# Kernel tuning notes

Hardware: AMD Instinct MI355X
Metric: run time of the kernel (lower is better)

Reference implementation:

```python
import jax, jax.numpy as jnp
import numpy as np

B, DIM, N = 8, 512, 1024
EMB, CDIM, M = 128, 512, 256
HEADS, DHEAD = 8, 64
DFF = 4 * DIM  # GEGLU inner dim


def _group_norm(x, g, b, groups=32, eps=1e-6):
    # x: [B, C, L]
    Bx, C, L = x.shape
    xr = x.reshape(Bx, groups, (C // groups) * L)
    mu = xr.mean(-1, keepdims=True)
    var = xr.var(-1, keepdims=True)
    xn = ((xr - mu) * jax.lax.rsqrt(var + eps)).reshape(Bx, C, L)
    return xn * g[None, :, None] + b[None, :, None]


def _layer_norm(x, g, b, eps=1e-5):
    mu = x.mean(-1, keepdims=True)
    var = x.var(-1, keepdims=True)
    return (x - mu) * jax.lax.rsqrt(var + eps) * g + b


def _attention(x, ctx, wq, wk, wv, wo, bo, heads):
    # x: [B, Nq, Dq], ctx: [B, Nk, Dk]
    Bx, Nq, _ = x.shape
    q = x @ wq.T
    k = ctx @ wk.T
    v = ctx @ wv.T
    d = q.shape[-1] // heads
    sp = lambda t: t.reshape(Bx, -1, heads, d).transpose(0, 2, 1, 3)  # b h n d
    q, k, v = sp(q), sp(k), sp(v)
    sim = jnp.einsum('bhid,bhjd->bhij', q, k) * (d ** -0.5)
    o = jnp.einsum('bhij,bhjd->bhid', jax.nn.softmax(sim, axis=-1), v)
    o = o.transpose(0, 2, 1, 3).reshape(Bx, Nq, heads * d)
    return o @ wo.T + bo


def setup_inputs() -> dict:
    key = jax.random.key(0)
    ks = jax.random.split(key, 16)
    rn = lambda k, sh: jax.random.normal(k, sh, dtype=jnp.float32) * 0.02
    inner = HEADS * DHEAD
    z = lambda n: jnp.zeros((n,), jnp.float32)
    o = lambda n: jnp.ones((n,), jnp.float32)
    return {
        'x': jax.random.normal(ks[0], (B, DIM, N), dtype=jnp.float32),
        'emb': jax.random.normal(ks[1], (B, EMB), dtype=jnp.float32),
        'context': jax.random.normal(ks[2], (B, CDIM, M), dtype=jnp.float32),
        'w_emb': rn(ks[3], (2 * DIM, EMB)), 'b_emb': z(2 * DIM),
        'gn_g': o(DIM), 'gn_b': z(DIM),
        'conv_w': rn(ks[4], (DIM, DIM)), 'conv_b': z(DIM),
        'a1_wq': rn(ks[5], (inner, DIM)), 'a1_wk': rn(ks[6], (inner, DIM)),
        'a1_wv': rn(ks[7], (inner, DIM)), 'a1_wo': rn(ks[8], (DIM, inner)), 'a1_bo': z(DIM),
        'a2_wq': rn(ks[9], (inner, DIM)), 'a2_wk': rn(ks[10], (inner, CDIM)),
        'a2_wv': rn(ks[11], (inner, CDIM)), 'a2_wo': rn(ks[12], (DIM, inner)), 'a2_bo': z(DIM),
        'ln1_g': o(DIM), 'ln1_b': z(DIM),
        'ln2_g': o(DIM), 'ln2_b': z(DIM),
        'ln3_g': o(DIM), 'ln3_b': z(DIM),
        'ff_w1': rn(ks[13], (2 * DFF, DIM)), 'ff_b1': z(2 * DFF),
        'ff_w2': rn(ks[14], (DIM, DFF)), 'ff_b2': z(DIM),
    }


def reference(x, emb, context, w_emb, b_emb, gn_g, gn_b, conv_w, conv_b,
              a1_wq, a1_wk, a1_wv, a1_wo, a1_bo,
              a2_wq, a2_wk, a2_wv, a2_wo, a2_bo,
              ln1_g, ln1_b, ln2_g, ln2_b, ln3_g, ln3_b,
              ff_w1, ff_b1, ff_w2, ff_b2):
    # scale-shift modulated GroupNorm + SiLU + 1x1 Conv1d residual branch
    emb_out = (jax.nn.silu(emb) @ w_emb.T + b_emb)[:, :, None]  # [B, 2*dim, 1]
    scale, shift = jnp.split(emb_out, 2, axis=1)
    h = _group_norm(x, gn_g, gn_b) * (1.0 + scale) + shift
    h = jnp.einsum('oc,bcn->bon', conv_w, jax.nn.silu(h)) + conv_b[None, :, None]
    x = x + h
    # to token-major layout
    xt = x.transpose(0, 2, 1)          # [B, N, dim]
    ctx = context.transpose(0, 2, 1)   # [B, M, context_dim]
    # self attention
    y = _layer_norm(xt, ln1_g, ln1_b)
    xt = _attention(y, y, a1_wq, a1_wk, a1_wv, a1_wo, a1_bo, HEADS) + xt
    # cross attention
    xt = _attention(_layer_norm(xt, ln2_g, ln2_b), ctx,
                    a2_wq, a2_wk, a2_wv, a2_wo, a2_bo, HEADS) + xt
    # GEGLU feed-forward
    u = _layer_norm(xt, ln3_g, ln3_b) @ ff_w1.T + ff_b1
    a, g = jnp.split(u, 2, axis=-1)
    xt = (a * jax.nn.gelu(g, approximate=False)) @ ff_w2.T + ff_b2 + xt
    return xt.transpose(0, 2, 1)  # back to [B, dim, N]
```

## Files before the change

kernel.cpp:

```cpp
#include <hip/hip_runtime.h>
#include <math.h>

#define NB 8
#define CDIM 512
#define NT 1024
#define MT 256
#define DFFI 2048

typedef short bf16x8 __attribute__((ext_vector_type(8)));
typedef float f32x4 __attribute__((ext_vector_type(4)));

__device__ __forceinline__ float sigmoidf_(float v){ return 1.0f/(1.0f+__expf(-v)); }

__device__ __forceinline__ short f2bf(float f){
    union { float f; unsigned u; } v; v.f = f;
    unsigned r = v.u + 0x7FFFu + ((v.u >> 16) & 1u);
    return (short)(r >> 16);
}

#define GLDS(gp, lp) __builtin_amdgcn_global_load_lds( \
    (const __attribute__((address_space(1))) void*)(gp), \
    (__attribute__((address_space(3))) void*)(lp), 16, 0, 0)

__global__ void cvt_all(const float* __restrict__ a1wq, const float* __restrict__ a1wk,
                        const float* __restrict__ a1wv, const float* __restrict__ a1wo,
                        const float* __restrict__ a2wq, const float* __restrict__ a2wk,
                        const float* __restrict__ a2wv, const float* __restrict__ a2wo,
                        const float* __restrict__ ffw1, const float* __restrict__ ffw2,
                        const float* __restrict__ convw, short* __restrict__ WB){
    int e = (blockIdx.x*256 + threadIdx.x)*8;
    if (e >= 5505024) return;
    const float* src; int off;
    if (e < 2097152){
        const float* tbl[8] = {a1wq,a1wk,a1wv,a1wo,a2wq,a2wk,a2wv,a2wo};
        src = tbl[e >> 18]; off = e & 262143;
    } else if (e < 4194304){ src = ffw1; off = e - 2097152; }
    else if (e < 5242880){ src = ffw2; off = e - 4194304; }
    else { src = convw; off = e - 5242880; }
    float4 x0 = ((const float4*)(src+off))[0], x1 = ((const float4*)(src+off))[1];
    bf16x8 v;
    v[0]=f2bf(x0.x); v[1]=f2bf(x0.y); v[2]=f2bf(x0.z); v[3]=f2bf(x0.w);
    v[4]=f2bf(x1.x); v[5]=f2bf(x1.y); v[6]=f2bf(x1.z); v[7]=f2bf(x1.w);
    *(bf16x8*)(WB + e) = v;
}


__global__ void emb_gemm(const float* __restrict__ emb, const float* __restrict__ w,
                         const float* __restrict__ bias, float* __restrict__ out){
    int idx = blockIdx.x*256 + threadIdx.x;
    int b = idx >> 10, o = idx & 1023;
    const float* e = emb + b*128;
    const float* wr = w + (size_t)o*128;
    float acc = 0.f;
    for (int i=0;i<128;i++){ float ev=e[i]; acc += (ev*sigmoidf_(ev))*wr[i]; }
    out[idx] = acc + bias[o];
}

__global__ void gn_stats(const float* __restrict__ x, float* __restrict__ stats){
    int bg = blockIdx.x;
    const float* base = x + (size_t)bg*16*NT;
    float s=0.f, sq=0.f;
    for (int i=threadIdx.x; i<16*NT; i+=256){ float v = base[i]; s+=v; sq+=v*v; }
    __shared__ float rs[256], rq[256];
    rs[threadIdx.x]=s; rq[threadIdx.x]=sq; __syncthreads();
    for (int st=128; st>0; st>>=1){
        if (threadIdx.x<st){ rs[threadIdx.x]+=rs[threadIdx.x+st]; rq[threadIdx.x]+=rq[threadIdx.x+st]; }
        __syncthreads();
    }
    if (threadIdx.x==0){
        float mu = rs[0]/(16.f*NT);
        float var = rq[0]/(16.f*NT) - mu*mu;
        stats[2*bg] = mu; stats[2*bg+1] = rsqrtf(var + 1e-6f);
    }
}

__global__ void mod_act(const float* __restrict__ x, const float* __restrict__ stats,
                        const float* __restrict__ gg, const float* __restrict__ gb,
                        const float* __restrict__ ss, short* __restrict__ act_t){
    __shared__ float tile[32][33];
    int n0 = blockIdx.x*32, c0 = blockIdx.y*32, b = blockIdx.z;
    int tx = threadIdx.x, ty = threadIdx.y;
    #pragma unroll
    for (int k=0;k<4;k++){
        int c = c0 + ty + k*8;
        tile[ty+k*8][tx] = x[((size_t)(b*CDIM+c))*NT + n0 + tx];
    }
    __syncthreads();
    #pragma unroll
    for (int k=0;k<4;k++){
        int c = c0 + tx, n = n0 + ty + k*8;
        float raw = tile[tx][ty+k*8];
        int gi = b*32 + (c>>4);
        float v = (raw - stats[2*gi]) * stats[2*gi+1] * gg[c] + gb[c];
        v = v * (1.f + ss[b*1024 + c]) + ss[b*1024 + 512 + c];
        act_t[((size_t)(b*NT+n))*CDIM + c] = f2bf(v * sigmoidf_(v));
    }
}

__global__ void ln_rows(const float* __restrict__ in, const float* __restrict__ g,
                        const float* __restrict__ bta, short* __restrict__ out){
    int row = blockIdx.x*4 + (threadIdx.x>>6);
    int lane = threadIdx.x & 63;
    const float* base = in + (size_t)row*CDIM + lane*8;
    float4 a = ((const float4*)base)[0], b4 = ((const float4*)base)[1];
    float vals[8] = {a.x,a.y,a.z,a.w,b4.x,b4.y,b4.z,b4.w};
    float s = 0.f, q = 0.f;
    #pragma unroll
    for (int i=0;i<8;i++){ s += vals[i]; q += vals[i]*vals[i]; }
    #pragma unroll
    for (int off=32; off>0; off>>=1){ s += __shfl_xor(s, off); q += __shfl_xor(q, off); }
    float mu = s*(1.f/512.f);
    float rstd = rsqrtf(q*(1.f/512.f) - mu*mu + 1e-5f);
    const float* gp = g + lane*8;
    const float* bp = bta + lane*8;
    float4 g0=((const float4*)gp)[0], g1=((const float4*)gp)[1];
    float4 e0=((const float4*)bp)[0], e1=((const float4*)bp)[1];
    float gs[8] = {g0.x,g0.y,g0.z,g0.w,g1.x,g1.y,g1.z,g1.w};
    float es[8] = {e0.x,e0.y,e0.z,e0.w,e1.x,e1.y,e1.z,e1.w};
    bf16x8 o8;
    #pragma unroll
    for (int i=0;i<8;i++) o8[i] = f2bf((vals[i]-mu)*rstd*gs[i] + es[i]);
    *(bf16x8*)(out + (size_t)row*CDIM + lane*8) = o8;
}

__global__ void transpose_ctx(const float* __restrict__ in, short* __restrict__ out){
    __shared__ float tile[32][33];
    int m0 = blockIdx.x*32, c0 = blockIdx.y*32, b = blockIdx.z;
    int tx=threadIdx.x, ty=threadIdx.y;
    #pragma unroll
    for (int k=0;k<4;k++){
        int c = c0+ty+k*8;
        tile[ty+k*8][tx] = in[((size_t)(b*512+c))*MT + m0+tx];
    }
    __syncthreads();
    #pragma unroll
    for (int k=0;k<4;k++){
        int m = m0+ty+k*8, c = c0+tx;
        out[((size_t)(b*MT+m))*512 + c] = f2bf(tile[tx][ty+k*8]);
    }
}

__global__ void transpose_out(const float* __restrict__ in, float* __restrict__ out){
    __shared__ float tile[32][33];
    int n0 = blockIdx.x*32, c0 = blockIdx.y*32, b=blockIdx.z;
    int tx=threadIdx.x, ty=threadIdx.y;
    #pragma unroll
    for (int k=0;k<4;k++){
        int n = n0+ty+k*8;
        tile[ty+k*8][tx] = in[((size_t)(b*NT+n))*512 + c0+tx];
    }
    __syncthreads();
    #pragma unroll
    for (int k=0;k<4;k++){
        int c = c0+ty+k*8, n = n0+tx;
        out[((size_t)(b*512+c))*NT + n] = tile[tx][ty+k*8];
    }
}

__global__ __launch_bounds__(256,2) void gemm_bb(
        const short* __restrict__ A, const short* __restrict__ W,
        const float* __restrict__ bias, const float* __restrict__ res,
        float* __restrict__ outf, short* __restrict__ outb,
        int K, int O, int ostr, int resmode){
    __shared__ short As[2][128*64];
    __shared__ short Bs[2][64*64];
    int r0 = blockIdx.x*128, o0 = blockIdx.y*64;
    int tid = threadIdx.x, w = tid>>6, lane = tid&63;
    int quad = lane>>4, lw = lane&15;
    int g_row = lane>>3, g_s = lane&7;
    int sseg = g_s ^ g_row;
    int wr = (w&1)*64, wc = (w>>1)*32;
    const short* Abase = A + (size_t)r0*K;
    const short* Wbase = W + (size_t)o0*K;
    f32x4 acc[4][2] = {};

    auto issue = [&](int buf, int kk){
        #pragma unroll
        for (int j=0;j<4;j++){
            int row = w*32 + j*8 + g_row;
            GLDS(Abase + (size_t)row*K + kk + sseg*8, &As[buf][(w*32+j*8)*64]);
        }
        #pragma unroll
        for (int j=0;j<2;j++){
            int row = w*16 + j*8 + g_row;
            GLDS(Wbase + (size_t)row*K + kk + sseg*8, &Bs[buf][(w*16+j*8)*64]);
        }
    };

    issue(0, 0);
    int nk = K >> 6;
    for (int it=0; it<nk; ++it){
        int cur = it & 1;
        if (it+1 < nk){
            issue(cur^1, (it+1)<<6);
            __asm__ volatile("s_waitcnt vmcnt(6)" ::: "memory");
        } else {
            __asm__ volatile("s_waitcnt vmcnt(0)" ::: "memory");
        }
        __builtin_amdgcn_s_barrier();
        bf16x8 af[4][2], bf[2][2];
        #pragma unroll
        for (int ks=0; ks<2; ks++){
            #pragma unroll
            for (int i=0;i<4;i++){
                int row = wr + i*16 + lw;
                af[i][ks] = *(const bf16x8*)&As[cur][row*64 + (((ks*4+quad) ^ (lw&7)))*8];
            }
            #pragma unroll
            for (int j=0;j<2;j++){
                int col = wc + j*16 + lw;
                bf[j][ks] = *(const bf16x8*)&Bs[cur][col*64 + (((ks*4+quad) ^ (lw&7)))*8];
            }
        }
        #pragma unroll
        for (int ks=0; ks<2; ks++)
            #pragma unroll
            for (int i=0;i<4;i++)
                #pragma unroll
                for (int j=0;j<2;j++)
                    acc[i][j] = __builtin_amdgcn_mfma_f32_16x16x32_bf16(af[i][ks], bf[j][ks], acc[i][j], 0, 0, 0);
        __asm__ volatile("s_waitcnt lgkmcnt(0)" ::: "memory");
        __builtin_amdgcn_s_barrier();
    }
    #pragma unroll
    for (int i=0;i<4;i++){
        #pragma unroll
        for (int j=0;j<2;j++){
            #pragma unroll
            for (int reg=0; reg<4; reg++){
                int row = r0 + wr + i*16 + quad*4 + reg;
                int col = o0 + wc + j*16 + lw;
                float v = acc[i][j][reg];
                if (bias) v += bias[col];
                if (resmode==1) v += res[(size_t)row*O + col];
                else if (resmode==2){
                    int b = row >> 10, n = row & 1023;
                    v += res[((size_t)(b*CDIM+col))*NT + n];
                }
                if (outf) outf[(size_t)row*ostr + col] = v;
                else      outb[(size_t)row*ostr + col] = f2bf(v);
            }
        }
    }
}

__global__ __launch_bounds__(256,2) void ff1_geglu_bb(
        const short* __restrict__ A, const short* __restrict__ W,
        const float* __restrict__ b1, short* __restrict__ out){
    __shared__ short As[128*64];
    __shared__ short Ba[64*64];
    __shared__ short Bg[64*64];
    int r0 = blockIdx.x*128, j0 = blockIdx.y*64;
    int tid = threadIdx.x, w = tid>>6, lane = tid&63;
    int quad = lane>>4, lw = lane&15;
    int g_row = lane>>3, g_s = lane&7;
    int sseg = g_s ^ g_row;
    int wr = (w&1)*64, wc = (w>>1)*32;
    f32x4 acca[4][2] = {}, accg[4][2] = {};
    for (int k0 = 0; k0 < 512; k0 += 64){
        #pragma unroll
        for (int j=0;j<4;j++){
            int row = w*32 + j*8 + g_row;
            GLDS(A + (size_t)(r0+row)*512 + k0 + sseg*8, As + (w*32+j*8)*64);
        }
        #pragma unroll
        for (int j=0;j<2;j++){
            int row = w*16 + j*8 + g_row;
            GLDS(W + (size_t)(j0+row)*512 + k0 + sseg*8, Ba + (w*16+j*8)*64);
            GLDS(W + (size_t)(2048+j0+row)*512 + k0 + sseg*8, Bg + (w*16+j*8)*64);
        }
        __syncthreads();
        bf16x8 af[4][2], ba[2][2], bg[2][2];
        #pragma unroll
        for (int ks=0; ks<2; ks++){
            #pragma unroll
            for (int i=0;i<4;i++){
                int row = wr + i*16 + lw;
                af[i][ks] = *(const bf16x8*)&As[row*64 + (((ks*4+quad) ^ (lw&7)))*8];
            }
            #pragma unroll
            for (int j=0;j<2;j++){
                int col = wc + j*16 + lw;
                ba[j][ks] = *(const bf16x8*)&Ba[col*64 + (((ks*4+quad) ^ (lw&7)))*8];
                bg[j][ks] = *(const bf16x8*)&Bg[col*64 + (((ks*4+quad) ^ (lw&7)))*8];
            }
        }
        #pragma unroll
        for (int ks=0; ks<2; ks++)
            #pragma unroll
            for (int i=0;i<4;i++)
                #pragma unroll
                for (int j=0;j<2;j++){
                    acca[i][j] = __builtin_amdgcn_mfma_f32_16x16x32_bf16(af[i][ks], ba[j][ks], acca[i][j], 0, 0, 0);
                    accg[i][j] = __builtin_amdgcn_mfma_f32_16x16x32_bf16(af[i][ks], bg[j][ks], accg[i][j], 0, 0, 0);
                }
        __syncthreads();
    }
    #pragma unroll
    for (int i=0;i<4;i++){
        #pragma unroll
        for (int j=0;j<2;j++){
            #pragma unroll
            for (int reg=0; reg<4; reg++){
                int row = r0 + wr + i*16 + quad*4 + reg;
                int col = j0 + wc + j*16 + lw;
                float a = acca[i][j][reg] + b1[col];
                float g = accg[i][j][reg] + b1[2048+col];
                float gl = 0.5f*g*(1.0f + erff(g*0.70710678118654752f));
                out[(size_t)row*DFFI + col] = f2bf(a*gl);
            }
        }
    }
}

__global__ __launch_bounds__(256) void attn_fa(
        const short* __restrict__ q, const short* __restrict__ k,
        const short* __restrict__ vt, short* __restrict__ o,
        int Nq, int Nk, int qstr, int kstr, int vtstr, float sc_log2e){
    __shared__ short Ks[64*64];
    __shared__ short Vs[64*64];
    __shared__ short QP[64*64];
    int bh = blockIdx.x & 63;
    int qt = blockIdx.x >> 6;
    int b = bh >> 3, h = bh & 7;
    int tid = threadIdx.x, w = tid>>6, lane = tid&63;
    int quad = lane>>4, lw = lane&15;
    int lrow = lane>>3, lg = (lane&7) ^ (lane>>3);
    int q0 = qt*64;

    #pragma unroll
    for (int t=0;t<2;t++){
        int row = w*16 + t*8 + lrow;
        GLDS(q + (size_t)(b*Nq + q0 + row)*qstr + h*64 + lg*8, QP + (w*16+t*8)*64);
    }
    __syncthreads();
    bf16x8 qf[2];
    {
        int r = w*16 + lw;
        qf[0] = *(const bf16x8*)&QP[r*64 + (( quad      ^ (r&7))*8)];
        qf[1] = *(const bf16x8*)&QP[r*64 + (((quad+4) ^ (r&7))*8)];
    }

    f32x4 oacc[4] = {};
    f32x4 accl = {};
    bf16x8 ones;
    #pragma unroll
    for (int i=0;i<8;i++) ones[i] = (short)0x3F80;

    int nkt = Nk >> 6;
    for (int kt = 0; kt < nkt; kt++){
        __syncthreads();
        #pragma unroll
        for (int t=0;t<2;t++){
            int row = w*16 + t*8 + lrow;
            GLDS(k  + (size_t)(b*Nk + kt*64 + row)*kstr + h*64 + lg*8, Ks + (w*16+t*8)*64);
            GLDS(vt + (size_t)(h*64 + row)*vtstr + b*Nk + kt*64 + lg*8, Vs + (w*16+t*8)*64);
        }
        __syncthreads();

        f32x4 s[4] = {};
        #pragma unroll
        for (int ct=0;ct<4;ct++){
            int r = ct*16 + lw;
            bf16x8 kf0 = *(const bf16x8*)&Ks[r*64 + (( quad      ^ (r&7))*8)];
            bf16x8 kf1 = *(const bf16x8*)&Ks[r*64 + (((quad+4) ^ (r&7))*8)];
            s[ct] = __builtin_amdgcn_mfma_f32_16x16x32_bf16(qf[0], kf0, s[ct], 0,0,0);
            s[ct] = __builtin_amdgcn_mfma_f32_16x16x32_bf16(qf[1], kf1, s[ct], 0,0,0);
        }

        #pragma unroll
        for (int ct=0;ct<4;ct++){
            int colb = (((ct+quad)&3)*16) + lw;
            #pragma unroll
            for (int r=0;r<4;r++){
                float p = exp2f(s[ct][r]*sc_log2e);
                union { float f; unsigned u; } uv; uv.f = p;
                QP[(w*16 + quad*4 + r)*64 + colb] = (short)(uv.u >> 16);
            }
        }
        __asm__ volatile("s_waitcnt lgkmcnt(0)" ::: "memory");

        bf16x8 pf[2];
        {
            int r = w*16 + lw;
            int rot = (lw>>2)&3;
            pf[0] = *(const bf16x8*)&QP[r*64 + (((    (quad>>1) + rot)&3)*16) + (quad&1)*8];
            pf[1] = *(const bf16x8*)&QP[r*64 + (((2 + (quad>>1) + rot)&3)*16) + (quad&1)*8];
        }
        accl = __builtin_amdgcn_mfma_f32_16x16x32_bf16(pf[0], ones, accl, 0,0,0);
        accl = __builtin_amdgcn_mfma_f32_16x16x32_bf16(pf[1], ones, accl, 0,0,0);
        #pragma unroll
        for (int dt=0; dt<4; dt++){
            int r = dt*16 + lw;
            bf16x8 vf0 = *(const bf16x8*)&Vs[r*64 + (( quad      ^ (r&7))*8)];
            bf16x8 vf1 = *(const bf16x8*)&Vs[r*64 + (((quad+4) ^ (r&7))*8)];
            oacc[dt] = __builtin_amdgcn_mfma_f32_16x16x32_bf16(pf[0], vf0, oacc[dt], 0,0,0);
            oacc[dt] = __builtin_amdgcn_mfma_f32_16x16x32_bf16(pf[1], vf1, oacc[dt], 0,0,0);
        }
    }
    float inv[4];
    #pragma unroll
    for (int r=0;r<4;r++) inv[r] = 1.0f/accl[r];
    #pragma unroll
    for (int dt=0; dt<4; dt++){
        #pragma unroll
        for (int r=0;r<4;r++){
            int qi = q0 + w*16 + quad*4 + r;
            o[(size_t)(b*Nq + qi)*512 + h*64 + dt*16 + lw] = f2bf(oacc[dt][r]*inv[r]);
        }
    }
}

extern "C" void kernel_launch(void* const* d_in, const int* in_sizes, int n_in,
                              void* d_out, int out_size, void* d_ws, size_t ws_size,
                              hipStream_t stream) {
    const float* x      = (const float*)d_in[0];
    const float* emb    = (const float*)d_in[1];
    const float* context= (const float*)d_in[2];
    const float* w_emb  = (const float*)d_in[3];
    const float* b_emb  = (const float*)d_in[4];
    const float* gn_g   = (const float*)d_in[5];
    const float* gn_b   = (const float*)d_in[6];
    const float* conv_w = (const float*)d_in[7];
    const float* conv_b = (const float*)d_in[8];
    const float* a1_wq  = (const float*)d_in[9];
    const float* a1_wk  = (const float*)d_in[10];
    const float* a1_wv  = (const float*)d_in[11];
    const float* a1_wo  = (const float*)d_in[12];
    const float* a1_bo  = (const float*)d_in[13];
    const float* a2_wq  = (const float*)d_in[14];
    const float* a2_wk  = (const float*)d_in[15];
    const float* a2_wv  = (const float*)d_in[16];
    const float* a2_wo  = (const float*)d_in[17];
    const float* a2_bo  = (const float*)d_in[18];
    const float* ln1_g  = (const float*)d_in[19];
    const float* ln1_b  = (const float*)d_in[20];
    const float* ln2_g  = (const float*)d_in[21];
    const float* ln2_b  = (const float*)d_in[22];
    const float* ln3_g  = (const float*)d_in[23];
    const float* ln3_b  = (const float*)d_in[24];
    const float* ff_w1  = (const float*)d_in[25];
    const float* ff_b1  = (const float*)d_in[26];
    const float* ff_w2  = (const float*)d_in[27];
    const float* ff_b2  = (const float*)d_in[28];
    float* out = (float*)d_out;

    char* base = (char*)d_ws;
    float* SS    = (float*)base;
    float* STATS = SS + 8192;
    float* F0    = (float*)(base + 65536);
    float* F1    = F0 + 4194304;
    short* WB    = (short*)(F1 + 4194304);
    short* qkW   = WB;
    short* vW    = WB + 524288;
    short* wo1W  = WB + 786432;
    short* a2qW  = WB + 1048576;
    short* a2kW  = WB + 1310720;
    short* a2vW  = WB + 1572864;
    short* wo2W  = WB + 1835008;
    short* ffw1W = WB + 2097152;
    short* ffw2W = WB + 4194304;
    short* convW = WB + 5242880;
    short* CTXb  = WB + 5505024;
    short* L0    = CTXb + 1048576;
    short* BIG   = L0 + 4194304;
    short* Q0    = BIG;
    short* VT1   = BIG + 8388608;
    short* AO    = BIG + 12582912;
    short* A2Q   = BIG;
    short* K2    = BIG + 4194304;
    short* VT2   = BIG + 5242880;
    short* ACT2  = BIG;

    dim3 tb(32,8);
    const float SCL2E = 0.125f * 1.4426950408889634f;

    cvt_all<<<2688,256,0,stream>>>(a1_wq,a1_wk,a1_wv,a1_wo,a2_wq,a2_wk,a2_wv,a2_wo,
                                   ff_w1,ff_w2,conv_w, WB);

    emb_gemm<<<32,256,0,stream>>>(emb, w_emb, b_emb, SS);
    gn_stats<<<256,256,0,stream>>>(x, STATS);
    mod_act<<<dim3(32,16,8), tb, 0, stream>>>(x, STATS, gn_g, gn_b, SS, L0);
    transpose_ctx<<<dim3(8,16,8), tb, 0, stream>>>(context, CTXb);
    gemm_bb<<<dim3(64,8),256,0,stream>>>(L0, convW, conv_b, x, F0, nullptr, 512, 512, 512, 2);

    ln_rows<<<2048,256,0,stream>>>(F0, ln1_g, ln1_b, L0);
    gemm_bb<<<dim3(64,16),256,0,stream>>>(L0, qkW, nullptr, nullptr, nullptr, Q0, 512, 1024, 1024, 0);
    gemm_bb<<<dim3(4,128),256,0,stream>>>(vW, L0, nullptr, nullptr, nullptr, VT1, 512, 8192, 8192, 0);
    attn_fa<<<1024,256,0,stream>>>(Q0, Q0+512, VT1, AO, 1024, 1024, 1024, 1024, 8192, SCL2E);
    gemm_bb<<<dim3(64,8),256,0,stream>>>(AO, wo1W, a1_bo, F0, F1, nullptr, 512, 512, 512, 1);

    ln_rows<<<2048,256,0,stream>>>(F1, ln2_g, ln2_b, L0);
    gemm_bb<<<dim3(64,8),256,0,stream>>>(L0, a2qW, nullptr, nullptr, nullptr, A2Q, 512, 512, 512, 0);
    gemm_bb<<<dim3(16,8),256,0,stream>>>(CTXb, a2kW, nullptr, nullptr, nullptr, K2, 512, 512, 512, 0);
    gemm_bb<<<dim3(4,32),256,0,stream>>>(a2vW, CTXb, nullptr, nullptr, nullptr, VT2, 512, 2048, 2048, 0);
    attn_fa<<<1024,256,0,stream>>>(A2Q, K2, VT2, AO, 1024, 256, 512, 512, 2048, SCL2E);
    gemm_bb<<<dim3(64,8),256,0,stream>>>(AO, wo2W, a2_bo, F1, F0, nullptr, 512, 512, 512, 1);

    ln_rows<<<2048,256,0,stream>>>(F0, ln3_g, ln3_b, L0);
    ff1_geglu_bb<<<dim3(64,32),256,0,stream>>>(L0, ffw1W, ff_b1, ACT2);
    gemm_bb<<<dim3(64,8),256,0,stream>>>(ACT2, ffw2W, ff_b2, F0, F1, nullptr, 2048, 512, 512, 1);
    transpose_out<<<dim3(32,16,8), tb, 0, stream>>>(F1, out);
}
```

Before: 469.8 us.

## Add 64x64-tile GEMM for narrow outputs and drop double buffering in gemm_bb

Adds a gemm64 kernel with 64x64 output tiles and uses it for the 512-wide projection GEMMs, doubling block count so more CUs are busy on these small problems. gemm_bb loses its double-buffered global_load_lds pipeline and becomes a single-buffer load/sync/compute loop, so loads no longer overlap with MFMA work. The smaller tiles give less data reuse per block, and the remaining gemm_bb (QK projection) may slow down without prefetch.

```diff
diff --git a/kernel.cpp b/kernel.cpp
--- a/kernel.cpp
+++ b/kernel.cpp
@@ -162,54 +162,39 @@
         const float* __restrict__ bias, const float* __restrict__ res,
         float* __restrict__ outf, short* __restrict__ outb,
         int K, int O, int ostr, int resmode){
-    __shared__ short As[2][128*64];
-    __shared__ short Bs[2][64*64];
+    __shared__ short As[128*64];
+    __shared__ short Bs[64*64];
     int r0 = blockIdx.x*128, o0 = blockIdx.y*64;
     int tid = threadIdx.x, w = tid>>6, lane = tid&63;
     int quad = lane>>4, lw = lane&15;
     int g_row = lane>>3, g_s = lane&7;
     int sseg = g_s ^ g_row;
     int wr = (w&1)*64, wc = (w>>1)*32;
-    const short* Abase = A + (size_t)r0*K;
-    const short* Wbase = W + (size_t)o0*K;
     f32x4 acc[4][2] = {};
-
-    auto issue = [&](int buf, int kk){
+    for (int k0 = 0; k0 < K; k0 += 64){
         #pragma unroll
         for (int j=0;j<4;j++){
             int row = w*32 + j*8 + g_row;
-            GLDS(Abase + (size_t)row*K + kk + sseg*8, &As[buf][(w*32+j*8)*64]);
+            GLDS(A + (size_t)(r0+row)*K + k0 + sseg*8, As + (w*32+j*8)*64);
         }
         #pragma unroll
         for (int j=0;j<2;j++){
             int row = w*16 + j*8 + g_row;
-            GLDS(Wbase + (size_t)row*K + kk + sseg*8, &Bs[buf][(w*16+j*8)*64]);
-        }
-    };
-
-    issue(0, 0);
-    int nk = K >> 6;
-    for (int it=0; it<nk; ++it){
-        int cur = it & 1;
-        if (it+1 < nk){
-            issue(cur^1, (it+1)<<6);
-            __asm__ volatile("s_waitcnt vmcnt(6)" ::: "memory");
-        } else {
-            __asm__ volatile("s_waitcnt vmcnt(0)" ::: "memory");
-        }
-        __builtin_amdgcn_s_barrier();
+            GLDS(W + (size_t)(o0+row)*K + k0 + sseg*8, Bs + (w*16+j*8)*64);
+        }
+        __syncthreads();
         bf16x8 af[4][2], bf[2][2];
         #pragma unroll
         for (int ks=0; ks<2; ks++){
             #pragma unroll
             for (int i=0;i<4;i++){
                 int row = wr + i*16 + lw;
-                af[i][ks] = *(const bf16x8*)&As[cur][row*64 + (((ks*4+quad) ^ (lw&7)))*8];
+                af[i][ks] = *(const bf16x8*)&As[row*64 + (((ks*4+quad) ^ (lw&7)))*8];
             }
             #pragma unroll
             for (int j=0;j<2;j++){
                 int col = wc + j*16 + lw;
-                bf[j][ks] = *(const bf16x8*)&Bs[cur][col*64 + (((ks*4+quad) ^ (lw&7)))*8];
+                bf[j][ks] = *(const bf16x8*)&Bs[col*64 + (((ks*4+quad) ^ (lw&7)))*8];
             }
         }
         #pragma unroll
@@ -219,11 +204,73 @@
                 #pragma unroll
                 for (int j=0;j<2;j++)
                     acc[i][j] = __builtin_amdgcn_mfma_f32_16x16x32_bf16(af[i][ks], bf[j][ks], acc[i][j], 0, 0, 0);
-        __asm__ volatile("s_waitcnt lgkmcnt(0)" ::: "memory");
-        __builtin_amdgcn_s_barrier();
+        __syncthreads();
     }
     #pragma unroll
     for (int i=0;i<4;i++){
+        #pragma unroll
+        for (int j=0;j<2;j++){
+            #pragma unroll
+            for (int reg=0; reg<4; reg++){
+                int row = r0 + wr + i*16 + quad*4 + reg;
+                int col = o0 + wc + j*16 + lw;
+                float v = acc[i][j][reg];
+                if (bias) v += bias[col];
+                if (resmode==1) v += res[(size_t)row*O + col];
+                else if (resmode==2){
+                    int b = row >> 10, n = row & 1023;
+                    v += res[((size_t)(b*CDIM+col))*NT + n];
+                }
+                if (outf) outf[(size_t)row*ostr + col] = v;
+                else      outb[(size_t)row*ostr + col] = f2bf(v);
+            }
+        }
+    }
+}
+
+__global__ __launch_bounds__(256) void gemm64(
+        const short* __restrict__ A, const short* __restrict__ W,
+        const float* __restrict__ bias, const float* __restrict__ res,
+        float* __restrict__ outf, short* __restrict__ outb,
+        int K, int O, int ostr, int resmode){
+    __shared__ short As[64*64];
+    __shared__ short Bs[64*64];
+    int r0 = blockIdx.x*64, o0 = blockIdx.y*64;
+    int tid = threadIdx.x, w = tid>>6, lane = tid&63;
+    int quad = lane>>4, lw = lane&15;
+    int lrow = lane>>3, lg = (lane&7) ^ (lane>>3);
+    int wr = (w&1)*32, wc = (w>>1)*32;
+    f32x4 acc[2][2] = {};
+    for (int k0 = 0; k0 < K; k0 += 64){
+        #pragma unroll
+        for (int t=0;t<2;t++){
+            int row = w*16 + t*8 + lrow;
+            GLDS(A + (size_t)(r0+row)*K + k0 + lg*8, As + (w*16+t*8)*64);
+            GLDS(W + (size_t)(o0+row)*K + k0 + lg*8, Bs + (w*16+t*8)*64);
+        }
+        __syncthreads();
+        bf16x8 af[2][2], bf[2][2];
+        #pragma unroll
+        for (int ks=0; ks<2; ks++){
+            #pragma unroll
+            for (int i=0;i<2;i++){
+                int row = wr + i*16 + lw;
+                af[i][ks] = *(const bf16x8*)&As[row*64 + (((ks*4+quad) ^ (lw&7)))*8];
+                int col = wc + i*16 + lw;
+                bf[i][ks] = *(const bf16x8*)&Bs[col*64 + (((ks*4+quad) ^ (lw&7)))*8];
+            }
+        }
+        #pragma unroll
+        for (int ks=0; ks<2; ks++)
+            #pragma unroll
+            for (int i=0;i<2;i++)
+                #pragma unroll
+                for (int j=0;j<2;j++)
+                    acc[i][j] = __builtin_amdgcn_mfma_f32_16x16x32_bf16(af[i][ks], bf[j][ks], acc[i][j], 0, 0, 0);
+        __syncthreads();
+    }
+    #pragma unroll
+    for (int i=0;i<2;i++){
         #pragma unroll
         for (int j=0;j<2;j++){
             #pragma unroll
@@ -482,23 +529,23 @@
     gn_stats<<<256,256,0,stream>>>(x, STATS);
     mod_act<<<dim3(32,16,8), tb, 0, stream>>>(x, STATS, gn_g, gn_b, SS, L0);
     transpose_ctx<<<dim3(8,16,8), tb, 0, stream>>>(context, CTXb);
-    gemm_bb<<<dim3(64,8),256,0,stream>>>(L0, convW, conv_b, x, F0, nullptr, 512, 512, 512, 2);
+    gemm64<<<dim3(128,8),256,0,stream>>>(L0, convW, conv_b, x, F0, nullptr, 512, 512, 512, 2);
 
     ln_rows<<<2048,256,0,stream>>>(F0, ln1_g, ln1_b, L0);
     gemm_bb<<<dim3(64,16),256,0,stream>>>(L0, qkW, nullptr, nullptr, nullptr, Q0, 512, 1024, 1024, 0);
-    gemm_bb<<<dim3(4,128),256,0,stream>>>(vW, L0, nullptr, nullptr, nullptr, VT1, 512, 8192, 8192, 0);
+    gemm64<<<dim3(8,128),256,0,stream>>>(vW, L0, nullptr, nullptr, nullptr, VT1, 512, 8192, 8192, 0);
     attn_fa<<<1024,256,0,stream>>>(Q0, Q0+512, VT1, AO, 1024, 1024, 1024, 1024, 8192, SCL2E);
-    gemm_bb<<<dim3(64,8),256,0,stream>>>(AO, wo1W, a1_bo, F0, F1, nullptr, 512, 512, 512, 1);
+    gemm64<<<dim3(128,8),256,0,stream>>>(AO, wo1W, a1_bo, F0, F1, nullptr, 512, 512, 512, 1);
 
     ln_rows<<<2048,256,0,stream>>>(F1, ln2_g, ln2_b, L0);
-    gemm_bb<<<dim3(64,8),256,0,stream>>>(L0, a2qW, nullptr, nullptr, nullptr, A2Q, 512, 512, 512, 0);
-    gemm_bb<<<dim3(16,8),256,0,stream>>>(CTXb, a2kW, nullptr, nullptr, nullptr, K2, 512, 512, 512, 0);
-    gemm_bb<<<dim3(4,32),256,0,stream>>>(a2vW, CTXb, nullptr, nullptr, nullptr, VT2, 512, 2048, 2048, 0);
+    gemm64<<<dim3(128,8),256,0,stream>>>(L0, a2qW, nullptr, nullptr, nullptr, A2Q, 512, 512, 512, 0);
+    gemm64<<<dim3(32,8),256,0,stream>>>(CTXb, a2kW, nullptr, nullptr, nullptr, K2, 512, 512, 512, 0);
+    gemm64<<<dim3(8,32),256,0,stream>>>(a2vW, CTXb, nullptr, nullptr, nullptr, VT2, 512, 2048, 2048, 0);
     attn_fa<<<1024,256,0,stream>>>(A2Q, K2, VT2, AO, 1024, 256, 512, 512, 2048, SCL2E);
-    gemm_bb<<<dim3(64,8),256,0,stream>>>(AO, wo2W, a2_bo, F1, F0, nullptr, 512, 512, 512, 1);
+    gemm64<<<dim3(128,8),256,0,stream>>>(AO, wo2W, a2_bo, F1, F0, nullptr, 512, 512, 512, 1);
 
     ln_rows<<<2048,256,0,stream>>>(F0, ln3_g, ln3_b, L0);
     ff1_geglu_bb<<<dim3(64,32),256,0,stream>>>(L0, ffw1W, ff_b1, ACT2);
-    gemm_bb<<<dim3(64,8),256,0,stream>>>(ACT2, ffw2W, ff_b2, F0, F1, nullptr, 2048, 512, 512, 1);
+    gemm64<<<dim3(128,8),256,0,stream>>>(ACT2, ffw2W, ff_b2, F0, F1, nullptr, 2048, 512, 512, 1);
     transpose_out<<<dim3(32,16,8), tb, 0, stream>>>(F1, out);
 }
```

Result: faster. 441.7 us (-6.0%).
